# Performance work log

Measured on AMD Instinct MI355X. Metric: run time of the kernel, lower is better.

## Reference

```python
import jax, jax.numpy as jnp
import numpy as np

B, LAT, FCON, NCOND = 1024, 64, 256, 1
HID, E, GATE_H = 512, 8, 64
FREC, NFUT = 256, 2
IN_SZ = LAT + FCON * NCOND          # 320
INTER = LAT + HID                   # 576
OUT_SZ = NFUT * FREC                # 512


def setup_inputs() -> dict:
    key = jax.random.key(0)
    ks = jax.random.split(key, 16)

    def kaiming(k, shape):
        # kaiming_uniform over fan_in = shape[-2] (matches torch init on [E, in, out])
        fan_in = shape[-2]
        bound = np.sqrt(6.0 / fan_in)
        return jax.random.uniform(k, shape, jnp.float32, -bound, bound)

    def lin(kw, kb, din, dout):
        bound = 1.0 / np.sqrt(din)
        w = jax.random.uniform(kw, (din, dout), jnp.float32, -bound, bound)
        b = jax.random.uniform(kb, (dout,), jnp.float32, -bound, bound)
        return w, b

    gw1, gb1 = lin(ks[0], ks[1], IN_SZ, GATE_H)
    gw2, gb2 = lin(ks[2], ks[3], GATE_H, GATE_H)
    gw3, gb3 = lin(ks[4], ks[5], GATE_H, E)

    return {
        "z": jax.random.normal(ks[6], (B, LAT), jnp.float32),
        "c": jax.random.normal(ks[7], (B, FCON * NCOND), jnp.float32),
        "w0": kaiming(ks[8], (E, IN_SZ, HID)),
        "b0": jnp.full((E, HID), 0.01, jnp.float32),
        "w1": kaiming(ks[9], (E, INTER, HID)),
        "b1": jnp.full((E, HID), 0.01, jnp.float32),
        "w2": kaiming(ks[10], (E, INTER, OUT_SZ)),
        "b2": jnp.full((E, OUT_SZ), 0.01, jnp.float32),
        "gw1": gw1, "gb1": gb1,
        "gw2": gw2, "gb2": gb2,
        "gw3": gw3, "gb3": gb3,
    }


def _moe_layer(coeff, z, layer_out, w, b, act):
    # math identical to: mixed_w = coeff @ flat(w); baddbmm(mixed_b, inp, mixed_w)
    # expressed as a fused contraction (no [B, in, out] materialization)
    inp = jnp.concatenate((z, layer_out), axis=1)          # [B, in]
    out = jnp.einsum('bi,eio,be->bo', inp, w, coeff)       # [B, out]
    out = out + coeff @ b                                  # mixed bias
    return act(out) if act is not None else out


def reference(z, c, w0, b0, w1, b1, w2, b2, gw1, gb1, gw2, gb2, gw3, gb3):
    x = jnp.concatenate((z, c), axis=1)                    # [B, IN_SZ]
    h = jax.nn.elu(x @ gw1 + gb1)
    h = jax.nn.elu(h @ gw2 + gb2)
    coeff = jax.nn.softmax(h @ gw3 + gb3, axis=1)          # [B, E]

    out = _moe_layer(coeff, z, c, w0, b0, jax.nn.elu)      # [B, HID]
    out = _moe_layer(coeff, z, out, w1, b1, jax.nn.elu)    # [B, HID]
    out = _moe_layer(coeff, z, out, w2, b2, None)          # [B, OUT_SZ]
    return out
```

## Files before the change

kernel.cpp:

```cpp
#include <hip/hip_runtime.h>
#include <hip/hip_bf16.h>
#include <stdint.h>
#include <math.h>

#define B_    1024
#define LAT   64
#define FCON  256
#define IN_SZ 320
#define HID   512
#define E_    8
#define GH    64
#define INTER 576
#define OUT_SZ 512
#define NTOT  4096
#define KI0   10
#define KI12  18

typedef __attribute__((ext_vector_type(8))) __bf16 bf16x8;
typedef __attribute__((ext_vector_type(4))) float  f32x4;

__device__ __forceinline__ float elu_f(float x) { return x > 0.f ? x : expf(x) - 1.f; }
__device__ __forceinline__ __bf16 to_bf16(float f) {
    __hip_bfloat16 h = __float2bfloat16(f);
    return *reinterpret_cast<__bf16*>(&h);
}

__device__ __forceinline__ void async_ld16(const void* g, void* l) {
    __builtin_amdgcn_global_load_lds(
        (const __attribute__((address_space(1))) unsigned int*)g,
        (__attribute__((address_space(3))) unsigned int*)l,
        16, 0, 0);
}


#define SMEM_BYTES 32768
#define WPAD2 133

__device__ __forceinline__ void do_zcpack(
    int bx, const float* __restrict__ z, const float* __restrict__ c,
    bf16x8* __restrict__ Ap0, bf16x8* __restrict__ Ap1, bf16x8* __restrict__ Ap2)
{
    const int wid  = bx * 4 + (threadIdx.x >> 6);
    const int lane = threadIdx.x & 63, q = lane >> 4, r = lane & 15;
    bf16x8 v;
    if (wid < 128) {
        const int mi = wid >> 1, ki = wid & 1;
        const float* src = z + (size_t)(mi * 16 + r) * LAT + ki * 32 + q * 8;
        const f32x4 lo = *(const f32x4*)src, hi = *(const f32x4*)(src + 4);
#pragma unroll
        for (int j = 0; j < 4; j++) { v[j] = to_bf16(lo[j]); v[j + 4] = to_bf16(hi[j]); }
        Ap0[((size_t)mi * KI0  + ki) * 64 + lane] = v;
        Ap1[((size_t)mi * KI12 + ki) * 64 + lane] = v;
        Ap2[((size_t)mi * KI12 + ki) * 64 + lane] = v;
    } else {
        const int cid = wid - 128;
        const int mi = cid >> 3, ki = 2 + (cid & 7);
        const float* src = c + (size_t)(mi * 16 + r) * FCON + (ki - 2) * 32 + q * 8;
        const f32x4 lo = *(const f32x4*)src, hi = *(const f32x4*)(src + 4);
#pragma unroll
        for (int j = 0; j < 4; j++) { v[j] = to_bf16(lo[j]); v[j + 4] = to_bf16(hi[j]); }
        Ap0[((size_t)mi * KI0 + ki) * 64 + lane] = v;
    }
}

__device__ __forceinline__ void do_wpackh(
    int f, const float* __restrict__ w, bf16x8* __restrict__ Wp, int KI,
    float* __restrict__ lds)
{
    const int e = f / (KI * 4), rem = f % (KI * 4);
    const int ki = rem >> 2, oq = rem & 3;
    const int K = KI * 32;
    const float* base = w + ((size_t)e * K + ki * 32) * 512 + oq * 128;

#pragma unroll
    for (int p = 0; p < 4; ++p) {
        const int idx = p * 256 + threadIdx.x;
        const int kl = idx >> 5, c4 = idx & 31;
        const f32x4 v = *(const f32x4*)(base + (size_t)kl * 512 + c4 * 4);
        float* d = lds + kl * WPAD2 + c4 * 4;
        d[0] = v[0]; d[1] = v[1]; d[2] = v[2]; d[3] = v[3];
    }
    __syncthreads();

    const int wv = threadIdx.x >> 6, lane = threadIdx.x & 63;
    const int q = lane >> 4, r = lane & 15;
#pragma unroll
    for (int ff = 0; ff < 2; ++ff) {
        const int fo = wv * 2 + ff;
        const int ol = fo * 16 + r;
        bf16x8 v;
#pragma unroll
        for (int j = 0; j < 8; ++j) v[j] = to_bf16(lds[(q * 8 + j) * WPAD2 + ol]);
        const int ni = e * 32 + oq * 8 + fo;
        Wp[((size_t)ni * KI + ki) * 64 + lane] = v;
    }
}

__device__ __forceinline__ void do_gate(
    int bx, const float* __restrict__ z, const float* __restrict__ c,
    const float* __restrict__ gw1, const float* __restrict__ gb1,
    const float* __restrict__ gw2, const float* __restrict__ gb2,
    const float* __restrict__ gw3, const float* __restrict__ gb3,
    float* __restrict__ coeff, float* __restrict__ smem)
{
    float* xs = smem;
    float* h  = smem + 16 * 320;
    const int r0 = bx * 16;
    const int wave = threadIdx.x >> 6, lane = threadIdx.x & 63;

#pragma unroll
    for (int p = 0; p < 5; ++p) {
        const int idx = p * 256 + threadIdx.x;
        const int row = idx / 80, c4 = idx % 80;
        const float* src = (c4 < 16)
            ? (z + (size_t)(r0 + row) * LAT  + c4 * 4)
            : (c + (size_t)(r0 + row) * FCON + (c4 - 16) * 4);
        *(f32x4*)(xs + row * 320 + c4 * 4) = *(const f32x4*)src;
    }
    __syncthreads();

    float a0, a1, a2, a3;
    {
        const float b = gb1[lane];
        a0 = b; a1 = b; a2 = b; a3 = b;
        const float* x0 = xs + (wave * 4 + 0) * 320;
        const float* x1 = xs + (wave * 4 + 1) * 320;
        const float* x2 = xs + (wave * 4 + 2) * 320;
        const float* x3 = xs + (wave * 4 + 3) * 320;
#pragma unroll 8
        for (int i = 0; i < IN_SZ; ++i) {
            const float wv = gw1[i * GH + lane];
            a0 = fmaf(x0[i], wv, a0);
            a1 = fmaf(x1[i], wv, a1);
            a2 = fmaf(x2[i], wv, a2);
            a3 = fmaf(x3[i], wv, a3);
        }
        h[(wave * 4 + 0) * GH + lane] = elu_f(a0);
        h[(wave * 4 + 1) * GH + lane] = elu_f(a1);
        h[(wave * 4 + 2) * GH + lane] = elu_f(a2);
        h[(wave * 4 + 3) * GH + lane] = elu_f(a3);
    }
    {
        const float b = gb2[lane];
        a0 = b; a1 = b; a2 = b; a3 = b;
        const float* h0 = h + (wave * 4 + 0) * GH;
        const float* h1 = h + (wave * 4 + 1) * GH;
        const float* h2 = h + (wave * 4 + 2) * GH;
        const float* h3 = h + (wave * 4 + 3) * GH;
#pragma unroll 8
        for (int i = 0; i < GH; ++i) {
            const float wv = gw2[i * GH + lane];
            a0 = fmaf(h0[i], wv, a0);
            a1 = fmaf(h1[i], wv, a1);
            a2 = fmaf(h2[i], wv, a2);
            a3 = fmaf(h3[i], wv, a3);
        }
        h[(wave * 4 + 0) * GH + lane] = elu_f(a0);
        h[(wave * 4 + 1) * GH + lane] = elu_f(a1);
        h[(wave * 4 + 2) * GH + lane] = elu_f(a2);
        h[(wave * 4 + 3) * GH + lane] = elu_f(a3);
    }
    if (lane < 32) {
        const int rloc = lane >> 3, e = lane & 7;
        const float* hr = h + (wave * 4 + rloc) * GH;
        float lg = gb3[e];
#pragma unroll 8
        for (int i = 0; i < GH; ++i) lg = fmaf(hr[i], gw3[i * E_ + e], lg);
        float mx = lg;
        mx = fmaxf(mx, __shfl_xor(mx, 1, 8));
        mx = fmaxf(mx, __shfl_xor(mx, 2, 8));
        mx = fmaxf(mx, __shfl_xor(mx, 4, 8));
        const float ex = expf(lg - mx);
        float sm = ex;
        sm += __shfl_xor(sm, 1, 8);
        sm += __shfl_xor(sm, 2, 8);
        sm += __shfl_xor(sm, 4, 8);
        coeff[(size_t)(r0 + wave * 4 + rloc) * E_ + e] = ex / sm;
    }
}

template<int KI, int FINAL>
__device__ __forceinline__ void layer_body(
    int b, const bf16x8* __restrict__ Ap, const bf16x8* __restrict__ Wp,
    const float* __restrict__ coeff, const float* __restrict__ bias,
    __bf16* __restrict__ ApN, float* __restrict__ fout, bf16x8* bs)
{
    constexpr int NS = KI / 2;
    const int lane = threadIdx.x & 63, w = threadIdx.x >> 6;
    const int q = lane >> 4, r = lane & 15;
    const int nt = b & 31, by = b >> 5;
    const int o0 = nt * 16;
    const int mi = by * 4 + w;

    const bf16x8* aB = Ap + (size_t)mi * KI * 64 + lane;
    const int e0 = w * 2;

    f32x4 acc[E_];
#pragma unroll
    for (int e = 0; e < E_; e++) acc[e] = (f32x4){0.f, 0.f, 0.f, 0.f};

#define BSI(buf_, kk_, e_) (&bs[(((size_t)(buf_) * 2 + (kk_)) * E_ + (e_)) * 64])
#define STAGE(s_, buf_)                                                        \
    {                                                                          \
        _Pragma("unroll")                                                      \
        for (int kk = 0; kk < 2; ++kk) {                                       \
            _Pragma("unroll")                                                  \
            for (int t = 0; t < 2; ++t) {                                      \
                const int e = e0 + t;                                          \
                const bf16x8* g = Wp +                                         \
                    ((size_t)e * 32 * KI + (size_t)nt * KI + ((s_) * 2 + kk)) * 64 + lane; \
                async_ld16((const void*)g, (void*)BSI(buf_, kk, e));           \
            }                                                                  \
        }                                                                      \
    }

    STAGE(0, 0);
    bf16x8 af0 = aB[0], af1 = aB[64];
    __syncthreads();

    int cur = 0;
#pragma unroll
    for (int s = 0; s < NS; ++s) {
        bf16x8 afn0 = af0, afn1 = af1;
        if (s + 1 < NS) {
            STAGE(s + 1, cur ^ 1);
            afn0 = aB[(size_t)(s * 2 + 2) * 64];
            afn1 = aB[(size_t)(s * 2 + 3) * 64];
        }
#pragma unroll
        for (int kk = 0; kk < 2; ++kk) {
            const bf16x8 af = kk ? af1 : af0;
            bf16x8 bfr[E_];
#pragma unroll
            for (int e = 0; e < E_; e++) bfr[e] = *(BSI(cur, kk, e) + lane);
#pragma unroll
            for (int e = 0; e < E_; e++)
                acc[e] = __builtin_amdgcn_mfma_f32_16x16x32_bf16(af, bfr[e], acc[e], 0, 0, 0);
        }
        __syncthreads();
        af0 = afn0; af1 = afn1; cur ^= 1;
    }
#undef STAGE
#undef BSI

    float be[E_];
#pragma unroll
    for (int e = 0; e < E_; e++) be[e] = bias[(size_t)e * 512 + o0 + r];

#pragma unroll
    for (int v = 0; v < 4; v++) {
        const int row = mi * 16 + q * 4 + v;
        const float* cr = coeff + (size_t)row * E_;
        const f32x4 clo = *(const f32x4*)cr, chi = *(const f32x4*)(cr + 4);
        float sv = 0.f;
#pragma unroll
        for (int e = 0; e < 4; e++) sv += clo[e] * (acc[e][v] + be[e]);
#pragma unroll
        for (int e = 0; e < 4; e++) sv += chi[e] * (acc[4 + e][v] + be[4 + e]);
        if (FINAL) {
            fout[(size_t)row * OUT_SZ + o0 + r] = sv;
        } else {
            const float hh = elu_f(sv);
            const int k  = LAT + o0 + r;
            const int ki2 = k >> 5, kq2 = (k & 31) >> 3, jb2 = k & 7;
            ApN[(((size_t)mi * KI12 + ki2) * 64 + kq2 * 16 + (q * 4 + v)) * 8 + jb2] =
                to_bf16(hh);
        }
    }
}

#define D1_GATE 64
#define D1_ZC   (D1_GATE + 160)
#define D1_ALL  (D1_ZC + 8 * KI0 * 4)

__global__ __launch_bounds__(256, 4) void prep_kernel(
    const float* __restrict__ z, const float* __restrict__ c,
    const float* __restrict__ w0,
    const float* __restrict__ gw1, const float* __restrict__ gb1,
    const float* __restrict__ gw2, const float* __restrict__ gb2,
    const float* __restrict__ gw3, const float* __restrict__ gb3,
    bf16x8* __restrict__ Ap0, bf16x8* __restrict__ Ap1, bf16x8* __restrict__ Ap2,
    bf16x8* __restrict__ Wp0,
    float* __restrict__ coeff)
{
    __shared__ __align__(16) uint8_t smem[SMEM_BYTES];
    const int bx = blockIdx.x;
    if (bx < D1_GATE) {
        do_gate(bx, z, c, gw1, gb1, gw2, gb2, gw3, gb3, coeff, (float*)smem);
    } else if (bx < D1_ZC) {
        do_zcpack(bx - D1_GATE, z, c, Ap0, Ap1, Ap2);
    } else {
        do_wpackh(bx - D1_ZC, w0, Wp0, KI0, (float*)smem);
    }
}

template<int KI, int FINAL>
__global__ __launch_bounds__(256, 4) void layer_wpack_kernel(
    const bf16x8* __restrict__ Ap, const bf16x8* __restrict__ Wp,
    const float* __restrict__ coeff, const float* __restrict__ bias,
    __bf16* __restrict__ ApN, float* __restrict__ fout,
    const float* __restrict__ wsrc, bf16x8* __restrict__ WpN)
{
    __shared__ __align__(16) uint8_t smem[SMEM_BYTES];
    const int b = blockIdx.x;
    if (b < 512) {
        layer_body<KI, FINAL>(b, Ap, Wp, coeff, bias, ApN, fout, (bf16x8*)smem);
    } else {
        do_wpackh(b - 512, wsrc, WpN, KI12, (float*)smem);
    }
}

static inline size_t align256(size_t x) { return (x + 255) & ~(size_t)255; }

extern "C" void kernel_launch(void* const* d_in, const int* in_sizes, int n_in,
                              void* d_out, int out_size, void* d_ws, size_t ws_size,
                              hipStream_t stream)
{
    const float* z   = (const float*)d_in[0];
    const float* c   = (const float*)d_in[1];
    const float* w0  = (const float*)d_in[2];
    const float* b0  = (const float*)d_in[3];
    const float* w1  = (const float*)d_in[4];
    const float* b1  = (const float*)d_in[5];
    const float* w2  = (const float*)d_in[6];
    const float* b2  = (const float*)d_in[7];
    const float* gw1 = (const float*)d_in[8];
    const float* gb1 = (const float*)d_in[9];
    const float* gw2 = (const float*)d_in[10];
    const float* gb2 = (const float*)d_in[11];
    const float* gw3 = (const float*)d_in[12];
    const float* gb3 = (const float*)d_in[13];
    float* out = (float*)d_out;

    uint8_t* p = (uint8_t*)d_ws;
    bf16x8* Wp0 = (bf16x8*)p; p += align256((size_t)NTOT * IN_SZ * 2);
    bf16x8* Wp1 = (bf16x8*)p; p += align256((size_t)NTOT * INTER * 2);
    bf16x8* Wp2 = (bf16x8*)p; p += align256((size_t)NTOT * INTER * 2);
    bf16x8* Ap0 = (bf16x8*)p; p += align256((size_t)B_ * IN_SZ * 2);
    bf16x8* Ap1 = (bf16x8*)p; p += align256((size_t)B_ * INTER * 2);
    bf16x8* Ap2 = (bf16x8*)p; p += align256((size_t)B_ * INTER * 2);
    float* coeff = (float*)p; p += align256((size_t)B_ * E_ * 4);

    prep_kernel<<<D1_ALL, 256, 0, stream>>>(
        z, c, w0, gw1, gb1, gw2, gb2, gw3, gb3,
        Ap0, Ap1, Ap2, Wp0, coeff);

    layer_wpack_kernel<KI0, 0><<<512 + 8 * KI12 * 4, 256, 0, stream>>>(
        Ap0, Wp0, coeff, b0, (__bf16*)Ap1, nullptr, w1, Wp1);

    layer_wpack_kernel<KI12, 0><<<512 + 8 * KI12 * 4, 256, 0, stream>>>(
        Ap1, Wp1, coeff, b1, (__bf16*)Ap2, nullptr, w2, Wp2);

    layer_wpack_kernel<KI12, 1><<<512, 256, 0, stream>>>(
        Ap2, Wp2, coeff, b2, nullptr, out, nullptr, nullptr);
}
```

Measured before the change: 137.2 us.

## Deepen MoE layer GEMM pipeline to four LDS stages with explicit vmcnt waits

```diff
diff --git a/kernel.cpp b/kernel.cpp
--- a/kernel.cpp
+++ b/kernel.cpp
@@ -33,7 +33,7 @@
 }
 
 
-#define SMEM_BYTES 32768
+#define SMEM_PREP 32768
 #define WPAD2 133
 
 __device__ __forceinline__ void do_zcpack(
@@ -214,31 +214,38 @@
         }                                                                      \
     }
 
-    STAGE(0, 0);
-    bf16x8 af0 = aB[0], af1 = aB[64];
-    __syncthreads();
-
-    int cur = 0;
+    bf16x8 ap[4][2];
+    STAGE(0, 0); ap[0][0] = aB[0];      ap[0][1] = aB[64];
+    if (NS > 1) { STAGE(1, 1); ap[1][0] = aB[2 * 64]; ap[1][1] = aB[3 * 64]; }
+    if (NS > 2) { STAGE(2, 2); ap[2][0] = aB[4 * 64]; ap[2][1] = aB[5 * 64]; }
+
 #pragma unroll
     for (int s = 0; s < NS; ++s) {
-        bf16x8 afn0 = af0, afn1 = af1;
-        if (s + 1 < NS) {
-            STAGE(s + 1, cur ^ 1);
-            afn0 = aB[(size_t)(s * 2 + 2) * 64];
-            afn1 = aB[(size_t)(s * 2 + 3) * 64];
-        }
+        if (s + 2 < NS)      asm volatile("s_waitcnt vmcnt(12)" ::: "memory");
+        else if (s + 1 < NS) asm volatile("s_waitcnt vmcnt(6)"  ::: "memory");
+        else                 asm volatile("s_waitcnt vmcnt(0)"  ::: "memory");
+        __builtin_amdgcn_s_barrier();
+        __builtin_amdgcn_sched_barrier(0);
+
+        bf16x8 bfr[2][E_];
+#pragma unroll
+        for (int kk = 0; kk < 2; ++kk)
+#pragma unroll
+            for (int e = 0; e < E_; e++) bfr[kk][e] = *(BSI(s & 3, kk, e) + lane);
+
+        if (s + 3 < NS) {
+            STAGE(s + 3, (s + 3) & 3);
+            ap[(s + 3) & 3][0] = aB[(size_t)(2 * s + 6) * 64];
+            ap[(s + 3) & 3][1] = aB[(size_t)(2 * s + 7) * 64];
+        }
+
 #pragma unroll
         for (int kk = 0; kk < 2; ++kk) {
-            const bf16x8 af = kk ? af1 : af0;
-            bf16x8 bfr[E_];
-#pragma unroll
-            for (int e = 0; e < E_; e++) bfr[e] = *(BSI(cur, kk, e) + lane);
+            const bf16x8 af = ap[s & 3][kk];
 #pragma unroll
             for (int e = 0; e < E_; e++)
-                acc[e] = __builtin_amdgcn_mfma_f32_16x16x32_bf16(af, bfr[e], acc[e], 0, 0, 0);
-        }
-        __syncthreads();
-        af0 = afn0; af1 = afn1; cur ^= 1;
+                acc[e] = __builtin_amdgcn_mfma_f32_16x16x32_bf16(af, bfr[kk][e], acc[e], 0, 0, 0);
+        }
     }
 #undef STAGE
 #undef BSI
@@ -283,7 +290,7 @@
     bf16x8* __restrict__ Wp0,
     float* __restrict__ coeff)
 {
-    __shared__ __align__(16) uint8_t smem[SMEM_BYTES];
+    __shared__ __align__(16) uint8_t smem[SMEM_PREP];
     const int bx = blockIdx.x;
     if (bx < D1_GATE) {
         do_gate(bx, z, c, gw1, gb1, gw2, gb2, gw3, gb3, coeff, (float*)smem);
@@ -295,13 +302,13 @@
 }
 
 template<int KI, int FINAL>
-__global__ __launch_bounds__(256, 4) void layer_wpack_kernel(
+__global__ __launch_bounds__(256, 2) void layer_wpack_kernel(
     const bf16x8* __restrict__ Ap, const bf16x8* __restrict__ Wp,
     const float* __restrict__ coeff, const float* __restrict__ bias,
     __bf16* __restrict__ ApN, float* __restrict__ fout,
     const float* __restrict__ wsrc, bf16x8* __restrict__ WpN)
 {
-    __shared__ __align__(16) uint8_t smem[SMEM_BYTES];
+    __shared__ __align__(16) uint8_t smem[4 * 2 * E_ * 64 * 16];
     const int b = blockIdx.x;
     if (b < 512) {
         layer_body<KI, FINAL>(b, Ap, Wp, coeff, bias, ApN, fout, (bf16x8*)smem);
```

After: 137.9 us. About the same (+0.5%).
